# Kernel optimization log

Measured on AMD Instinct MI355X. Metric: run time of the kernel, lower is better.

The kernel has to match this reference:

```python
import jax, jax.numpy as jnp
import numpy as np

RPN_BATCH = 256
ROI_BATCH = 128
IMG = 800.0


def _box_iou(a, b):
    # a: [N,4], b: [G,4] -> [N,G]
    lt = jnp.maximum(a[:, None, :2], b[None, :, :2])
    rb = jnp.minimum(a[:, None, 2:], b[None, :, 2:])
    wh = jnp.clip(rb - lt, 0.0)
    inter = wh[..., 0] * wh[..., 1]
    area_a = (a[:, 2] - a[:, 0]) * (a[:, 3] - a[:, 1])
    area_b = (b[:, 2] - b[:, 0]) * (b[:, 3] - b[:, 1])
    return inter / (area_a[:, None] + area_b[None, :] - inter + 1e-6)


def _encode(a, t):
    wa = a[:, 2] - a[:, 0]
    ha = a[:, 3] - a[:, 1]
    xa = a[:, 0] + 0.5 * wa
    ya = a[:, 1] + 0.5 * ha
    wt = t[:, 2] - t[:, 0]
    ht = t[:, 3] - t[:, 1]
    xt = t[:, 0] + 0.5 * wt
    yt = t[:, 1] + 0.5 * ht
    return jnp.stack(((xt - xa) / wa, (yt - ya) / ha,
                      jnp.log(wt / wa + 1e-6), jnp.log(ht / ha + 1e-6)), axis=1)


def _smooth_l1(x):
    ax = jnp.abs(x)
    return jnp.where(ax < 1.0, 0.5 * x * x, ax - 0.5)


def _rpn_loss_one(scores, deltas, anchors, gt):
    # scores [N,1], deltas [N,4], anchors [N,4], gt [G,4]
    ious = _box_iou(anchors, gt)                 # [N,G]
    max_iou = ious.max(axis=1)
    argmax = ious.argmax(axis=1)
    labels = jnp.full((anchors.shape[0],), -1.0, dtype=scores.dtype)
    labels = jnp.where(max_iou < 0.3, 0.0, labels)
    labels = jnp.where(max_iou > 0.7, 1.0, labels)
    labels = labels.at[jnp.argmax(ious, axis=0)].set(1.0)  # each gt's best anchor is positive
    # deterministic subsampling: keep first K in index order (replaces randperm)
    num_pos = RPN_BATCH // 2
    pos = labels == 1.0
    labels = jnp.where(pos & (jnp.cumsum(pos) > num_pos), -1.0, labels)
    n_pos = jnp.sum(labels == 1.0)
    neg = labels == 0.0
    labels = jnp.where(neg & (jnp.cumsum(neg) > (RPN_BATCH - n_pos)), -1.0, labels)
    mask = (labels != -1.0).astype(scores.dtype)
    logit = scores[:, 0]
    t = jnp.clip(labels, 0.0, 1.0)
    bce = jnp.maximum(logit, 0.0) - logit * t + jnp.log1p(jnp.exp(-jnp.abs(logit)))
    cls = jnp.sum(bce * mask) / jnp.maximum(jnp.sum(mask), 1.0)
    tgt = _encode(anchors, gt[argmax])
    posm = (labels == 1.0).astype(scores.dtype)
    n_posf = jnp.sum(posm)
    reg = jnp.where(n_posf > 0,
                    jnp.sum(_smooth_l1(deltas - tgt) * posm[:, None])
                    / jnp.maximum(n_posf * 4.0, 1.0),
                    0.0)
    return cls + reg


def _det_loss_one(cls_scores, bbox_deltas, proposals, gt, gt_labels):
    # cls_scores [P,C], bbox_deltas [P,4C], proposals [P,4], gt [G,4], gt_labels [G]
    P = proposals.shape[0]
    ious = _box_iou(proposals, gt)
    max_iou = ious.max(axis=1)
    argmax = ious.argmax(axis=1)
    assigned = jnp.where(max_iou >= 0.5, gt_labels[argmax], 0)
    num_pos = ROI_BATCH // 4
    pos = assigned > 0
    pos_rank = jnp.cumsum(pos) - 1
    neg_rank = jnp.cumsum(~pos) - 1
    idx = jnp.arange(P)
    # sort key: first up-to-num_pos positives (index order), then negatives,
    # excess positives pushed to the end -> first ROI_BATCH entries are the sample
    key = jnp.where(pos,
                    jnp.where(pos_rank < num_pos, pos_rank, 2 * P + idx),
                    P + neg_rank)
    sampled = jnp.argsort(key)[:ROI_BATCH]
    t_labels = assigned[sampled]
    matched = gt[argmax[sampled]]
    t_deltas = _encode(proposals[sampled], matched)
    logp = jax.nn.log_softmax(cls_scores[sampled], axis=-1)
    cls = -jnp.mean(jnp.take_along_axis(logp, t_labels[:, None], axis=1)[:, 0])
    pd = bbox_deltas[sampled].reshape(ROI_BATCH, -1, 4)
    preds = pd[jnp.arange(ROI_BATCH), t_labels]  # class-specific deltas
    posm = (t_labels > 0).astype(cls_scores.dtype)
    n_pos = jnp.sum(posm)
    reg = jnp.where(n_pos > 0,
                    jnp.sum(_smooth_l1(preds - t_deltas) * posm[:, None])
                    / jnp.maximum(n_pos * 4.0, 1.0),
                    0.0)
    return cls + reg


def _rand_boxes(k, prefix):
    k1, k2 = jax.random.split(k)
    xy = jax.random.uniform(k1, prefix + (2,)) * (IMG - 130.0)
    wh = jax.random.uniform(k2, prefix + (2,)) * 120.0 + 8.0
    return jnp.concatenate([xy, xy + wh], axis=-1)


def setup_inputs() -> dict:
    B, N, P, G, C = 4, 250000, 1000, 32, 81
    key = jax.random.key(0)
    ks = jax.random.split(key, 8)
    return {
        "rpn_scores": jax.random.normal(ks[0], (B, N, 1), dtype=jnp.float32),
        "rpn_deltas": jax.random.normal(ks[1], (B, N, 4), dtype=jnp.float32) * 0.1,
        "cls_scores": jax.random.normal(ks[2], (B * P, C), dtype=jnp.float32),
        "bbox_deltas": jax.random.normal(ks[3], (B * P, 4 * C), dtype=jnp.float32) * 0.1,
        "anchors": _rand_boxes(ks[4], (N,)),
        "proposals": _rand_boxes(ks[5], (B, P)),
        "gt_boxes": _rand_boxes(ks[6], (B, G)),
        "gt_labels": jax.random.randint(ks[7], (B, G), 1, C, dtype=jnp.int32),
    }


def reference(rpn_scores, rpn_deltas, cls_scores, bbox_deltas,
              anchors, proposals, gt_boxes, gt_labels):
    B, P, _ = proposals.shape
    C = cls_scores.shape[-1]
    cls_b = cls_scores.reshape(B, P, C)
    del_b = bbox_deltas.reshape(B, P, 4 * C)
    rpn = jax.vmap(lambda s, d, g: _rpn_loss_one(s, d, anchors, g))(
        rpn_scores, rpn_deltas, gt_boxes)
    det = jax.vmap(_det_loss_one)(cls_b, del_b, proposals, gt_boxes, gt_labels)
    return jnp.sum(rpn) + jnp.sum(det)
```

## Files before the change

### kernel.cpp

```cpp
#include <hip/hip_runtime.h>
#include <math.h>
#include <stdint.h>

#define B_ 4
#define N_ 250000
#define P_ 1000
#define G_ 32
#define C_ 81
#define RPN_BATCH 256
#define ROI_BATCH 128

#define ABLK 1024
#define NBA ((N_ + ABLK - 1) / ABLK)

__device__ __forceinline__ float iou_one(float a0, float a1, float a2, float a3,
                                         float areaA,
                                         float b0, float b1, float b2, float b3) {
    float ltx = fmaxf(a0, b0), lty = fmaxf(a1, b1);
    float rbx = fminf(a2, b2), rby = fminf(a3, b3);
    float w = fmaxf(rbx - ltx, 0.f), h = fmaxf(rby - lty, 0.f);
    float inter = w * h;
    float areaB = (b2 - b0) * (b3 - b1);
    return inter / (areaA + areaB - inter + 1e-6f);
}

__device__ __forceinline__ unsigned long long shfl_xor_u64(unsigned long long v, int m) {
    unsigned lo = (unsigned)v, hi = (unsigned)(v >> 32);
    lo = __shfl_xor(lo, m);
    hi = __shfl_xor(hi, m);
    return ((unsigned long long)hi << 32) | lo;
}

__device__ __forceinline__ float smooth_l1(float x) {
    float ax = fabsf(x);
    return (ax < 1.f) ? 0.5f * x * x : ax - 0.5f;
}

__global__ void __launch_bounds__(256, 4) rpn_assign(
        const float* __restrict__ anchors, const float* __restrict__ gt_boxes,
        int8_t* __restrict__ labels, int* __restrict__ posCnt, int* __restrict__ negCnt,
        unsigned long long* __restrict__ blockBest,
        float* __restrict__ sums, float* __restrict__ out, int out_size) {
    __shared__ float4 sA[ABLK];
    __shared__ unsigned char sPart[4][ABLK];
    __shared__ int sCnt[8];

    int b = blockIdx.y, tid = threadIdx.x;
    int base = blockIdx.x * ABLK;

    if (blockIdx.x == 0 && b == 0) {
        if (tid < 8) sums[tid] = 0.f;
        for (int i = tid; i < out_size; i += 256) out[i] = 0.f;
    }

    for (int t = tid; t < ABLK; t += 256) {
        int ai = base + t;
        float4 v = make_float4(0.f, 0.f, 0.f, 0.f);
        if (ai < N_) v = ((const float4*)anchors)[ai];
        sA[t] = v;
    }
    __syncthreads();

    int lane = tid & 63, wave = tid >> 6;
    int waveu = __builtin_amdgcn_readfirstlane(wave);

    const float4* gt4 = (const float4*)gt_boxes + b * G_ + waveu * 8;
    float g0[8], g1[8], g2[8], g3[8], gae[8];
#pragma unroll
    for (int j = 0; j < 8; ++j) {
        float4 g = gt4[j];
        g0[j] = g.x; g1[j] = g.y; g2[j] = g.z; g3[j] = g.w;
        gae[j] = (g.z - g.x) * (g.w - g.y) + 1e-6f;
    }

    float bi[8], bd[8]; int bx[8];
#pragma unroll
    for (int j = 0; j < 8; ++j) { bi[j] = 0.f; bd[j] = 1.f; bx[j] = 0; }

    for (int k = 0; k < ABLK / 64; ++k) {
        int a = k * 64 + lane;
        float4 A = sA[a];
        float areaA = (A.z - A.x) * (A.w - A.y);
        int gidx = base + a;
        float acc03 = 1e30f, acc07 = 1e30f;
#pragma unroll
        for (int j = 0; j < 8; ++j) {
            float ltx = fmaxf(A.x, g0[j]), lty = fmaxf(A.y, g1[j]);
            float rbx = fminf(A.z, g2[j]), rby = fminf(A.w, g3[j]);
            float w = fmaxf(rbx - ltx, 0.f), h = fmaxf(rby - lty, 0.f);
            float inter = w * h;
            float d = (areaA + gae[j]) - inter;
            acc03 = fminf(acc03, fmaf(0.3f, d, -inter));
            acc07 = fminf(acc07, fmaf(0.7f, d, -inter));
            float p1 = inter * bd[j], p2 = bi[j] * d;
            if (p1 > p2) { bi[j] = inter; bd[j] = d; bx[j] = gidx; }
        }
        sPart[wave][a] = (unsigned char)(((acc07 < 0.f) ? 2 : 0) | ((acc03 > 0.f) ? 1 : 0));
    }

#pragma unroll
    for (int j = 0; j < 8; ++j) {
        float i_ = bi[j], d_ = bd[j]; int x_ = bx[j];
        for (int m = 32; m >= 1; m >>= 1) {
            float oi = __shfl_xor(i_, m), od = __shfl_xor(d_, m);
            int ox = __shfl_xor(x_, m);
            float pa = oi * d_, pb = i_ * od;
            bool take = (pa > pb) || (pa == pb && ox < x_);
            if (take) { i_ = oi; d_ = od; x_ = ox; }
        }
        if (lane == 0) {
            float iou = i_ / d_;
            unsigned long long pk =
                (((unsigned long long)__float_as_uint(iou)) << 32) |
                (unsigned)(0xFFFFFFFFu - (unsigned)x_);
            blockBest[((size_t)b * G_ + wave * 8 + j) * NBA + blockIdx.x] = pk;
        }
    }
    __syncthreads();

    unsigned u0 = ((const unsigned*)&sPart[0][0])[tid];
    unsigned u1 = ((const unsigned*)&sPart[1][0])[tid];
    unsigned u2 = ((const unsigned*)&sPart[2][0])[tid];
    unsigned u3 = ((const unsigned*)&sPart[3][0])[tid];
    unsigned andb = u0 & u1 & u2 & u3;
    unsigned orb  = u0 | u1 | u2 | u3;
    int gbase = base + tid * 4;
    unsigned outw = 0; int cp = 0, cn = 0;
#pragma unroll
    for (int j = 0; j < 4; ++j) {
        int above = (orb >> (8 * j + 1)) & 1;
        int below = (andb >> (8 * j)) & 1;
        int lab = above ? 1 : (below ? 0 : -1);
        if (gbase + j < N_) { cp += (lab == 1); cn += (lab == 0); }
        outw |= ((unsigned)(unsigned char)(char)lab) << (8 * j);
    }
    if (gbase < N_)
        ((unsigned*)labels)[(((size_t)b * N_ + base) >> 2) + tid] = outw;

    for (int m = 32; m >= 1; m >>= 1) { cp += __shfl_xor(cp, m); cn += __shfl_xor(cn, m); }
    if (lane == 0) { sCnt[wave] = cp; sCnt[4 + wave] = cn; }
    __syncthreads();
    if (tid == 0) {
        posCnt[b * NBA + blockIdx.x] = sCnt[0] + sCnt[1] + sCnt[2] + sCnt[3];
        negCnt[b * NBA + blockIdx.x] = sCnt[4] + sCnt[5] + sCnt[6] + sCnt[7];
    }
}

__global__ void __launch_bounds__(256) rpn_promote_scan(
        const unsigned long long* __restrict__ blockBest, int8_t* __restrict__ labels,
        int* __restrict__ posCnt, int* __restrict__ negCnt,
        int* __restrict__ totPos, int* __restrict__ totNeg) {
    int b = blockIdx.x, tid = threadIdx.x;
    __shared__ int sp[256], sn[256];
    __shared__ unsigned wIdx[G_];

    sp[tid] = (tid < NBA) ? posCnt[b * NBA + tid] : 0;
    sn[tid] = (tid < NBA) ? negCnt[b * NBA + tid] : 0;

    int g = tid >> 3, sub = tid & 7;
    unsigned long long v = 0;
    for (int j = sub; j < NBA; j += 8) {
        unsigned long long x = blockBest[((size_t)b * G_ + g) * NBA + j];
        if (x > v) v = x;
    }
    for (int m = 4; m >= 1; m >>= 1) {
        unsigned long long o = shfl_xor_u64(v, m);
        if (o > v) v = o;
    }
    if (sub == 0) wIdx[g] = 0xFFFFFFFFu - (unsigned)(v & 0xFFFFFFFFull);
    __syncthreads();
    if (tid < G_) {
        unsigned w = wIdx[tid];
        bool first = true;
        for (int j = 0; j < tid; ++j) if (wIdx[j] == w) first = false;
        if (first) {
            size_t li = (size_t)b * N_ + w;
            int8_t old = labels[li];
            labels[li] = 1;
            int blk = (int)(w / ABLK);
            if (old != 1) atomicAdd(&sp[blk], 1);
            if (old == 0) atomicAdd(&sn[blk], -1);
        }
    }
    __syncthreads();

    int vp = sp[tid], vn = sn[tid];
    for (int off = 1; off < 256; off <<= 1) {
        int tp = 0, tn = 0;
        if (tid >= off) { tp = sp[tid - off]; tn = sn[tid - off]; }
        __syncthreads();
        sp[tid] += tp; sn[tid] += tn;
        __syncthreads();
    }
    if (tid < NBA) {
        posCnt[b * NBA + tid] = sp[tid] - vp;
        negCnt[b * NBA + tid] = sn[tid] - vn;
    }
    if (tid == 0) { totPos[b] = sp[255]; totNeg[b] = sn[255]; }
}

__global__ void __launch_bounds__(256) rpn_sample(
        const int8_t* __restrict__ labels, const float* __restrict__ rpn_scores,
        const float* __restrict__ rpn_deltas, const float* __restrict__ anchors,
        const float* __restrict__ gt_boxes,
        const int* __restrict__ posBase, const int* __restrict__ negBase,
        const int* __restrict__ totPos, float* __restrict__ sums) {
    int b = blockIdx.y, tid = threadIdx.x;
    int base = blockIdx.x * ABLK;
    __shared__ float sg[G_ * 4];
    __shared__ int swP[4], swN[4];
    __shared__ float sred[8];
    if (tid < G_ * 4) sg[tid] = gt_boxes[b * G_ * 4 + tid];

    int gbase = base + tid * 4;
    unsigned word = 0xFFFFFFFFu;
    if (gbase < N_)
        word = ((const unsigned*)labels)[(((size_t)b * N_ + base) >> 2) + tid];
    int lab[4]; int cntP = 0, cntN = 0;
#pragma unroll
    for (int j = 0; j < 4; ++j) {
        lab[j] = (int)(char)((word >> (8 * j)) & 0xFF);
        cntP += (lab[j] == 1); cntN += (lab[j] == 0);
    }
    int lane = tid & 63, wave = tid >> 6;
    int ip = cntP, inn = cntN;
    for (int off = 1; off < 64; off <<= 1) {
        int vp = __shfl_up(ip, off), vn = __shfl_up(inn, off);
        if (lane >= off) { ip += vp; inn += vn; }
    }
    if (lane == 63) { swP[wave] = ip; swN[wave] = inn; }
    __syncthreads();
    int bP = 0, bN = 0;
    for (int w = 0; w < wave; ++w) { bP += swP[w]; bN += swN[w]; }
    int pP = posBase[b * NBA + blockIdx.x] + bP + ip - cntP;
    int pN = negBase[b * NBA + blockIdx.x] + bN + inn - cntN;

    int npos = min(totPos[b], RPN_BATCH / 2);
    int negQ = RPN_BATCH - npos;

    float bce = 0.f, regv = 0.f;
#pragma unroll
    for (int j = 0; j < 4; ++j) {
        int i = gbase + j;
        if (i >= N_) break;
        if (lab[j] == 1) {
            int r = pP++;
            if (r < RPN_BATCH / 2) {
                float l = rpn_scores[(size_t)b * N_ + i];
                bce += fmaxf(l, 0.f) - l + log1pf(expf(-fabsf(l)));
                float4 A = ((const float4*)anchors)[i];
                float areaA = (A.z - A.x) * (A.w - A.y);
                float best = -1.f; int am = 0;
                for (int g = 0; g < G_; ++g) {
                    float iou = iou_one(A.x, A.y, A.z, A.w, areaA,
                                        sg[g * 4], sg[g * 4 + 1], sg[g * 4 + 2], sg[g * 4 + 3]);
                    if (iou > best) { best = iou; am = g; }
                }
                float t0 = sg[am * 4], t1 = sg[am * 4 + 1], t2 = sg[am * 4 + 2], t3 = sg[am * 4 + 3];
                float wa = A.z - A.x, ha = A.w - A.y;
                float xa = A.x + 0.5f * wa, ya = A.y + 0.5f * ha;
                float wt = t2 - t0, ht = t3 - t1;
                float xt = t0 + 0.5f * wt, yt = t1 + 0.5f * ht;
                float4 D = ((const float4*)rpn_deltas)[(size_t)b * N_ + i];
                regv += smooth_l1(D.x - (xt - xa) / wa) + smooth_l1(D.y - (yt - ya) / ha) +
                        smooth_l1(D.z - logf(wt / wa + 1e-6f)) + smooth_l1(D.w - logf(ht / ha + 1e-6f));
            }
        } else if (lab[j] == 0) {
            int r = pN++;
            if (r < negQ) {
                float l = rpn_scores[(size_t)b * N_ + i];
                bce += fmaxf(l, 0.f) + log1pf(expf(-fabsf(l)));
            }
        }
    }
    for (int m = 32; m >= 1; m >>= 1) { bce += __shfl_xor(bce, m); regv += __shfl_xor(regv, m); }
    if (lane == 0) { sred[wave] = bce; sred[4 + wave] = regv; }
    __syncthreads();
    if (tid == 0) {
        float sb = sred[0] + sred[1] + sred[2] + sred[3];
        float sr = sred[4] + sred[5] + sred[6] + sred[7];
        if (sb != 0.f) atomicAdd(&sums[b], sb);
        if (sr != 0.f) atomicAdd(&sums[4 + b], sr);
    }
}

__global__ void __launch_bounds__(1024) det_all(
        const float* __restrict__ cls_scores, const float* __restrict__ bbox_deltas,
        const float* __restrict__ proposals, const float* __restrict__ gt_boxes,
        const int* __restrict__ gt_labels, const int* __restrict__ totPos,
        const int* __restrict__ totNeg, const float* __restrict__ sums,
        float* __restrict__ out) {
    int b = blockIdx.x, tid = threadIdx.x;
    int lane = tid & 63, wave = tid >> 6;
    __shared__ float sgt[G_ * 4];
    __shared__ int sgl[G_];
    __shared__ short sassign[P_];
    __shared__ unsigned char sargm[P_];
    __shared__ int sw[16];
    __shared__ int ssamp[ROI_BATCH];
    __shared__ float sRow[ROI_BATCH][C_];
    __shared__ float sM[ROI_BATCH], sLse[ROI_BATCH];
    __shared__ float cacc[2], racc[2];
    if (tid < G_ * 4) sgt[tid] = gt_boxes[b * G_ * 4 + tid];
    if (tid < G_) sgl[tid] = gt_labels[b * G_ + tid];
    __syncthreads();

    int lab = 0;
    if (tid < P_) {
        float4 A = ((const float4*)proposals)[b * P_ + tid];
        float areaA = (A.z - A.x) * (A.w - A.y);
        float best = -1.f; int am = 0;
#pragma unroll 8
        for (int g = 0; g < G_; ++g) {
            float iou = iou_one(A.x, A.y, A.z, A.w, areaA,
                                sgt[g * 4], sgt[g * 4 + 1], sgt[g * 4 + 2], sgt[g * 4 + 3]);
            if (iou > best) { best = iou; am = g; }
        }
        lab = (best >= 0.5f) ? sgl[am] : 0;
        sassign[tid] = (short)lab;
        sargm[tid] = (unsigned char)am;
    }

    int cnt = (tid < P_ && lab > 0) ? 1 : 0;
    int inc = cnt;
    for (int off = 1; off < 64; off <<= 1) {
        int v = __shfl_up(inc, off);
        if (lane >= off) inc += v;
    }
    if (lane == 63) sw[wave] = inc;
    __syncthreads();
    int basew = 0, total = 0;
    for (int w = 0; w < 16; ++w) { if (w < wave) basew += sw[w]; total += sw[w]; }
    int prefix = basew + inc - cnt;
    int npos_kept = min(total, ROI_BATCH / 4);
    int nneg_total = P_ - total;
    if (tid < P_) {
        int slot;
        if (lab > 0)
            slot = (prefix < ROI_BATCH / 4) ? prefix
                 : npos_kept + nneg_total + (prefix - ROI_BATCH / 4);
        else
            slot = npos_kept + (tid - prefix);
        if (slot < ROI_BATCH) ssamp[slot] = tid;
    }
    int np_det = npos_kept + max(0, ROI_BATCH - npos_kept - nneg_total);
    __syncthreads();

    for (int k = 0; k < 8; ++k) {
        int r = wave * 8 + k;
        int s = ssamp[r];
        const float* row = cls_scores + ((size_t)(b * P_ + s)) * C_;
        float v1 = row[lane];
        sRow[r][lane] = v1;
        if (lane < C_ - 64) sRow[r][64 + lane] = row[64 + lane];
    }
    __syncthreads();

    for (int k = 0; k < 8; ++k) {
        int r = wave * 8 + k;
        float v1 = sRow[r][lane];
        float v2 = (lane < C_ - 64) ? sRow[r][64 + lane] : -INFINITY;
        float m = fmaxf(v1, v2);
        for (int mm = 32; mm >= 1; mm >>= 1) m = fmaxf(m, __shfl_xor(m, mm));
        float se = expf(v1 - m) + ((lane < C_ - 64) ? expf(v2 - m) : 0.f);
        for (int mm = 32; mm >= 1; mm >>= 1) se += __shfl_xor(se, mm);
        if (lane == 0) { sM[r] = m; sLse[r] = logf(se); }
    }
    __syncthreads();

    float clsv = 0.f, regv = 0.f;
    if (tid < ROI_BATCH) {
        int s = ssamp[tid];
        int t = sassign[s];
        clsv = -(sRow[tid][t] - sM[tid] - sLse[tid]);
        if (t > 0) {
            int g = sargm[s];
            float4 A = ((const float4*)proposals)[b * P_ + s];
            float t0 = sgt[g * 4], t1 = sgt[g * 4 + 1];
            float t2 = sgt[g * 4 + 2], t3 = sgt[g * 4 + 3];
            float wa = A.z - A.x, ha = A.w - A.y;
            float xa = A.x + 0.5f * wa, ya = A.y + 0.5f * ha;
            float wt = t2 - t0, ht = t3 - t1;
            float xt = t0 + 0.5f * wt, yt = t1 + 0.5f * ht;
            const float4 pd = *(const float4*)(bbox_deltas +
                    ((size_t)(b * P_ + s)) * (4 * C_) + 4 * t);
            regv = smooth_l1(pd.x - (xt - xa) / wa) + smooth_l1(pd.y - (yt - ya) / ha) +
                   smooth_l1(pd.z - logf(wt / wa + 1e-6f)) + smooth_l1(pd.w - logf(ht / ha + 1e-6f));
        }
    }
    if (tid < 128) {
        for (int m = 32; m >= 1; m >>= 1) {
            clsv += __shfl_xor(clsv, m);
            regv += __shfl_xor(regv, m);
        }
        if (lane == 0) { cacc[wave] = clsv; racc[wave] = regv; }
    }
    __syncthreads();
    if (tid == 0) {
        float cls = (cacc[0] + cacc[1]) / (float)ROI_BATCH;
        float reg = (np_det > 0) ? (racc[0] + racc[1]) / fmaxf((float)np_det * 4.f, 1.f) : 0.f;
        int rnp = min(totPos[b], RPN_BATCH / 2);
        int kneg = min(totNeg[b], RPN_BATCH - rnp);
        float rcls = sums[b] / fmaxf((float)(rnp + kneg), 1.f);
        float rreg = (rnp > 0) ? sums[4 + b] / fmaxf((float)rnp * 4.f, 1.f) : 0.f;
        atomicAdd(out, cls + reg + rcls + rreg);
    }
}

extern "C" void kernel_launch(void* const* d_in, const int* in_sizes, int n_in,
                              void* d_out, int out_size, void* d_ws, size_t ws_size,
                              hipStream_t stream) {
    const float* rpn_scores  = (const float*)d_in[0];
    const float* rpn_deltas  = (const float*)d_in[1];
    const float* cls_scores  = (const float*)d_in[2];
    const float* bbox_deltas = (const float*)d_in[3];
    const float* anchors     = (const float*)d_in[4];
    const float* proposals   = (const float*)d_in[5];
    const float* gt_boxes    = (const float*)d_in[6];
    const int*   gt_labels   = (const int*)d_in[7];
    float* out = (float*)d_out;

    char* ws = (char*)d_ws;
    size_t off = 0;
    auto alloc = [&](size_t bytes) -> char* {
        size_t o = (off + 255) & ~(size_t)255;
        off = o + bytes;
        return ws + o;
    };
    int8_t* labels = (int8_t*)alloc((size_t)B_ * N_);
    unsigned long long* blockBest = (unsigned long long*)alloc((size_t)B_ * G_ * NBA * 8);
    int* posCnt = (int*)alloc((size_t)B_ * NBA * 4);
    int* negCnt = (int*)alloc((size_t)B_ * NBA * 4);
    int* totPos = (int*)alloc(B_ * 4);
    int* totNeg = (int*)alloc(B_ * 4);
    float* sums = (float*)alloc(8 * 4);

    rpn_assign<<<dim3(NBA, B_), 256, 0, stream>>>(anchors, gt_boxes, labels,
                                                  posCnt, negCnt, blockBest,
                                                  sums, out, out_size);
    rpn_promote_scan<<<B_, 256, 0, stream>>>(blockBest, labels, posCnt, negCnt,
                                             totPos, totNeg);
    rpn_sample<<<dim3(NBA, B_), 256, 0, stream>>>(labels, rpn_scores, rpn_deltas,
                                                  anchors, gt_boxes, posCnt, negCnt,
                                                  totPos, sums);
    det_all<<<B_, 1024, 0, stream>>>(cls_scores, bbox_deltas, proposals, gt_boxes,
                                     gt_labels, totPos, totNeg, sums, out);
}
```

Before: 159.0 us.

## Fold detection loss into RPN assign kernel as extra blocks, drop det_all launch

```diff
diff --git a/kernel.cpp b/kernel.cpp
--- a/kernel.cpp
+++ b/kernel.cpp
@@ -12,6 +12,7 @@
 
 #define ABLK 1024
 #define NBA ((N_ + ABLK - 1) / ABLK)
+#define DETB 4
 
 __device__ __forceinline__ float iou_one(float a0, float a1, float a2, float a3,
                                          float areaA,
@@ -36,20 +37,154 @@
     return (ax < 1.f) ? 0.5f * x * x : ax - 0.5f;
 }
 
-__global__ void __launch_bounds__(256, 4) rpn_assign(
+__global__ void __launch_bounds__(256, 4) rpn_assign_det(
         const float* __restrict__ anchors, const float* __restrict__ gt_boxes,
+        const int* __restrict__ gt_labels, const float* __restrict__ proposals,
+        const float* __restrict__ cls_scores, const float* __restrict__ bbox_deltas,
         int8_t* __restrict__ labels, int* __restrict__ posCnt, int* __restrict__ negCnt,
-        unsigned long long* __restrict__ blockBest,
-        float* __restrict__ sums, float* __restrict__ out, int out_size) {
+        unsigned long long* __restrict__ blockBest, float* __restrict__ detPart,
+        float* __restrict__ out, int out_size) {
+    int b = blockIdx.y, tid = threadIdx.x;
+    int lane = tid & 63, wave = tid >> 6;
+
+    if (blockIdx.x >= NBA) {
+        int h = blockIdx.x - NBA;
+        __shared__ float sgt[G_ * 4];
+        __shared__ int sgl[G_];
+        __shared__ short sassign[P_];
+        __shared__ unsigned char sargm[P_];
+        __shared__ int ssamp[ROI_BATCH];
+        __shared__ int swd[4];
+        __shared__ float sc[4], srg[4];
+        if (tid < G_ * 4) sgt[tid] = gt_boxes[b * G_ * 4 + tid];
+        if (tid < G_) sgl[tid] = gt_labels[b * G_ + tid];
+        __syncthreads();
+
+        int myPos = 0;
+        int labj[4];
+#pragma unroll
+        for (int j = 0; j < 4; ++j) {
+            int p = tid * 4 + j;
+            int labp = 0, am = 0;
+            if (p < P_) {
+                float4 A = ((const float4*)proposals)[b * P_ + p];
+                float areaA = (A.z - A.x) * (A.w - A.y);
+                float best = -1.f;
+#pragma unroll 8
+                for (int g = 0; g < G_; ++g) {
+                    float iou = iou_one(A.x, A.y, A.z, A.w, areaA,
+                                        sgt[g * 4], sgt[g * 4 + 1], sgt[g * 4 + 2], sgt[g * 4 + 3]);
+                    if (iou > best) { best = iou; am = g; }
+                }
+                labp = (best >= 0.5f) ? sgl[am] : 0;
+                sassign[p] = (short)labp;
+                sargm[p] = (unsigned char)am;
+                labj[j] = labp;
+                myPos += (labp > 0);
+            } else {
+                labj[j] = -1;
+            }
+        }
+
+        int inc = myPos;
+        for (int off = 1; off < 64; off <<= 1) {
+            int v = __shfl_up(inc, off);
+            if (lane >= off) inc += v;
+        }
+        if (lane == 63) swd[wave] = inc;
+        __syncthreads();
+        int basew = 0, total = 0;
+        for (int w = 0; w < 4; ++w) { if (w < wave) basew += swd[w]; total += swd[w]; }
+        int pp = basew + inc - myPos;
+        int npos_kept = min(total, ROI_BATCH / 4);
+        int nneg_total = P_ - total;
+#pragma unroll
+        for (int j = 0; j < 4; ++j) {
+            int p = tid * 4 + j;
+            if (labj[j] < 0) break;
+            int slot;
+            if (labj[j] > 0) {
+                slot = (pp < ROI_BATCH / 4) ? pp : npos_kept + nneg_total + (pp - ROI_BATCH / 4);
+                pp++;
+            } else {
+                slot = npos_kept + (p - pp);
+            }
+            if (slot < ROI_BATCH) ssamp[slot] = p;
+        }
+        int np_det = npos_kept + max(0, ROI_BATCH - npos_kept - nneg_total);
+        __syncthreads();
+
+        int rowBase = h * (ROI_BATCH / DETB) + wave * 8;
+        float clsAcc = 0.f;
+        for (int k = 0; k < 8; k += 2) {
+            int s0 = ssamp[rowBase + k], s1 = ssamp[rowBase + k + 1];
+            const float* r0 = cls_scores + ((size_t)(b * P_ + s0)) * C_;
+            const float* r1 = cls_scores + ((size_t)(b * P_ + s1)) * C_;
+            float a1 = r0[lane], b1 = r1[lane];
+            float a2 = (lane < C_ - 64) ? r0[64 + lane] : -INFINITY;
+            float b2 = (lane < C_ - 64) ? r1[64 + lane] : -INFINITY;
+            float m0 = fmaxf(a1, a2), m1 = fmaxf(b1, b2);
+            for (int mm = 32; mm >= 1; mm >>= 1) {
+                m0 = fmaxf(m0, __shfl_xor(m0, mm));
+                m1 = fmaxf(m1, __shfl_xor(m1, mm));
+            }
+            float e0 = expf(a1 - m0) + ((lane < C_ - 64) ? expf(a2 - m0) : 0.f);
+            float e1 = expf(b1 - m1) + ((lane < C_ - 64) ? expf(b2 - m1) : 0.f);
+            for (int mm = 32; mm >= 1; mm >>= 1) {
+                e0 += __shfl_xor(e0, mm);
+                e1 += __shfl_xor(e1, mm);
+            }
+            int t0 = sassign[s0], t1 = sassign[s1];
+            int q0 = (t0 < 64) ? t0 : t0 - 64;
+            int q1 = (t1 < 64) ? t1 : t1 - 64;
+            float lo0 = __shfl(a1, q0), hi0 = __shfl(a2, q0);
+            float lo1 = __shfl(b1, q1), hi1 = __shfl(b2, q1);
+            float v0 = (t0 < 64) ? lo0 : hi0;
+            float v1 = (t1 < 64) ? lo1 : hi1;
+            if (lane == 0)
+                clsAcc += -(v0 - m0 - logf(e0)) - (v1 - m1 - logf(e1));
+        }
+
+        float regAcc = 0.f;
+        if (lane < 8) {
+            int r = rowBase + lane;
+            int s = ssamp[r];
+            int t = sassign[s];
+            if (t > 0) {
+                int g = sargm[s];
+                float4 A = ((const float4*)proposals)[b * P_ + s];
+                float t0g = sgt[g * 4], t1g = sgt[g * 4 + 1];
+                float t2g = sgt[g * 4 + 2], t3g = sgt[g * 4 + 3];
+                float wa = A.z - A.x, ha = A.w - A.y;
+                float xa = A.x + 0.5f * wa, ya = A.y + 0.5f * ha;
+                float wt = t2g - t0g, ht = t3g - t1g;
+                float xt = t0g + 0.5f * wt, yt = t1g + 0.5f * ht;
+                const float4 pd = *(const float4*)(bbox_deltas +
+                        ((size_t)(b * P_ + s)) * (4 * C_) + 4 * t);
+                regAcc = smooth_l1(pd.x - (xt - xa) / wa) + smooth_l1(pd.y - (yt - ya) / ha) +
+                         smooth_l1(pd.z - logf(wt / wa + 1e-6f)) +
+                         smooth_l1(pd.w - logf(ht / ha + 1e-6f));
+            }
+        }
+        for (int mm = 32; mm >= 1; mm >>= 1) regAcc += __shfl_xor(regAcc, mm);
+        if (lane == 0) { sc[wave] = clsAcc; srg[wave] = regAcc; }
+        __syncthreads();
+        if (tid == 0) {
+            float cp = sc[0] + sc[1] + sc[2] + sc[3];
+            float rp = srg[0] + srg[1] + srg[2] + srg[3];
+            detPart[b * DETB + h] = cp / (float)ROI_BATCH +
+                ((np_det > 0) ? rp / fmaxf((float)np_det * 4.f, 1.f) : 0.f);
+        }
+        return;
+    }
+
     __shared__ float4 sA[ABLK];
     __shared__ unsigned char sPart[4][ABLK];
     __shared__ int sCnt[8];
 
-    int b = blockIdx.y, tid = threadIdx.x;
     int base = blockIdx.x * ABLK;
 
     if (blockIdx.x == 0 && b == 0) {
-        if (tid < 8) sums[tid] = 0.f;
         for (int i = tid; i < out_size; i += 256) out[i] = 0.f;
     }
 
@@ -61,7 +196,6 @@
     }
     __syncthreads();
 
-    int lane = tid & 63, wave = tid >> 6;
     int waveu = __builtin_amdgcn_readfirstlane(wave);
 
     const float4* gt4 = (const float4*)gt_boxes + b * G_ + waveu * 8;
@@ -204,7 +338,8 @@
         const float* __restrict__ rpn_deltas, const float* __restrict__ anchors,
         const float* __restrict__ gt_boxes,
         const int* __restrict__ posBase, const int* __restrict__ negBase,
-        const int* __restrict__ totPos, float* __restrict__ sums) {
+        const int* __restrict__ totPos, const int* __restrict__ totNeg,
+        const float* __restrict__ detPart, float* __restrict__ out) {
     int b = blockIdx.y, tid = threadIdx.x;
     int base = blockIdx.x * ABLK;
     __shared__ float sg[G_ * 4];
@@ -279,131 +414,15 @@
     if (tid == 0) {
         float sb = sred[0] + sred[1] + sred[2] + sred[3];
         float sr = sred[4] + sred[5] + sred[6] + sred[7];
-        if (sb != 0.f) atomicAdd(&sums[b], sb);
-        if (sr != 0.f) atomicAdd(&sums[4 + b], sr);
-    }
-}
-
-__global__ void __launch_bounds__(1024) det_all(
-        const float* __restrict__ cls_scores, const float* __restrict__ bbox_deltas,
-        const float* __restrict__ proposals, const float* __restrict__ gt_boxes,
-        const int* __restrict__ gt_labels, const int* __restrict__ totPos,
-        const int* __restrict__ totNeg, const float* __restrict__ sums,
-        float* __restrict__ out) {
-    int b = blockIdx.x, tid = threadIdx.x;
-    int lane = tid & 63, wave = tid >> 6;
-    __shared__ float sgt[G_ * 4];
-    __shared__ int sgl[G_];
-    __shared__ short sassign[P_];
-    __shared__ unsigned char sargm[P_];
-    __shared__ int sw[16];
-    __shared__ int ssamp[ROI_BATCH];
-    __shared__ float sRow[ROI_BATCH][C_];
-    __shared__ float sM[ROI_BATCH], sLse[ROI_BATCH];
-    __shared__ float cacc[2], racc[2];
-    if (tid < G_ * 4) sgt[tid] = gt_boxes[b * G_ * 4 + tid];
-    if (tid < G_) sgl[tid] = gt_labels[b * G_ + tid];
-    __syncthreads();
-
-    int lab = 0;
-    if (tid < P_) {
-        float4 A = ((const float4*)proposals)[b * P_ + tid];
-        float areaA = (A.z - A.x) * (A.w - A.y);
-        float best = -1.f; int am = 0;
-#pragma unroll 8
-        for (int g = 0; g < G_; ++g) {
-            float iou = iou_one(A.x, A.y, A.z, A.w, areaA,
-                                sgt[g * 4], sgt[g * 4 + 1], sgt[g * 4 + 2], sgt[g * 4 + 3]);
-            if (iou > best) { best = iou; am = g; }
-        }
-        lab = (best >= 0.5f) ? sgl[am] : 0;
-        sassign[tid] = (short)lab;
-        sargm[tid] = (unsigned char)am;
-    }
-
-    int cnt = (tid < P_ && lab > 0) ? 1 : 0;
-    int inc = cnt;
-    for (int off = 1; off < 64; off <<= 1) {
-        int v = __shfl_up(inc, off);
-        if (lane >= off) inc += v;
-    }
-    if (lane == 63) sw[wave] = inc;
-    __syncthreads();
-    int basew = 0, total = 0;
-    for (int w = 0; w < 16; ++w) { if (w < wave) basew += sw[w]; total += sw[w]; }
-    int prefix = basew + inc - cnt;
-    int npos_kept = min(total, ROI_BATCH / 4);
-    int nneg_total = P_ - total;
-    if (tid < P_) {
-        int slot;
-        if (lab > 0)
-            slot = (prefix < ROI_BATCH / 4) ? prefix
-                 : npos_kept + nneg_total + (prefix - ROI_BATCH / 4);
-        else
-            slot = npos_kept + (tid - prefix);
-        if (slot < ROI_BATCH) ssamp[slot] = tid;
-    }
-    int np_det = npos_kept + max(0, ROI_BATCH - npos_kept - nneg_total);
-    __syncthreads();
-
-    for (int k = 0; k < 8; ++k) {
-        int r = wave * 8 + k;
-        int s = ssamp[r];
-        const float* row = cls_scores + ((size_t)(b * P_ + s)) * C_;
-        float v1 = row[lane];
-        sRow[r][lane] = v1;
-        if (lane < C_ - 64) sRow[r][64 + lane] = row[64 + lane];
-    }
-    __syncthreads();
-
-    for (int k = 0; k < 8; ++k) {
-        int r = wave * 8 + k;
-        float v1 = sRow[r][lane];
-        float v2 = (lane < C_ - 64) ? sRow[r][64 + lane] : -INFINITY;
-        float m = fmaxf(v1, v2);
-        for (int mm = 32; mm >= 1; mm >>= 1) m = fmaxf(m, __shfl_xor(m, mm));
-        float se = expf(v1 - m) + ((lane < C_ - 64) ? expf(v2 - m) : 0.f);
-        for (int mm = 32; mm >= 1; mm >>= 1) se += __shfl_xor(se, mm);
-        if (lane == 0) { sM[r] = m; sLse[r] = logf(se); }
-    }
-    __syncthreads();
-
-    float clsv = 0.f, regv = 0.f;
-    if (tid < ROI_BATCH) {
-        int s = ssamp[tid];
-        int t = sassign[s];
-        clsv = -(sRow[tid][t] - sM[tid] - sLse[tid]);
-        if (t > 0) {
-            int g = sargm[s];
-            float4 A = ((const float4*)proposals)[b * P_ + s];
-            float t0 = sgt[g * 4], t1 = sgt[g * 4 + 1];
-            float t2 = sgt[g * 4 + 2], t3 = sgt[g * 4 + 3];
-            float wa = A.z - A.x, ha = A.w - A.y;
-            float xa = A.x + 0.5f * wa, ya = A.y + 0.5f * ha;
-            float wt = t2 - t0, ht = t3 - t1;
-            float xt = t0 + 0.5f * wt, yt = t1 + 0.5f * ht;
-            const float4 pd = *(const float4*)(bbox_deltas +
-                    ((size_t)(b * P_ + s)) * (4 * C_) + 4 * t);
-            regv = smooth_l1(pd.x - (xt - xa) / wa) + smooth_l1(pd.y - (yt - ya) / ha) +
-                   smooth_l1(pd.z - logf(wt / wa + 1e-6f)) + smooth_l1(pd.w - logf(ht / ha + 1e-6f));
-        }
-    }
-    if (tid < 128) {
-        for (int m = 32; m >= 1; m >>= 1) {
-            clsv += __shfl_xor(clsv, m);
-            regv += __shfl_xor(regv, m);
-        }
-        if (lane == 0) { cacc[wave] = clsv; racc[wave] = regv; }
-    }
-    __syncthreads();
-    if (tid == 0) {
-        float cls = (cacc[0] + cacc[1]) / (float)ROI_BATCH;
-        float reg = (np_det > 0) ? (racc[0] + racc[1]) / fmaxf((float)np_det * 4.f, 1.f) : 0.f;
         int rnp = min(totPos[b], RPN_BATCH / 2);
         int kneg = min(totNeg[b], RPN_BATCH - rnp);
-        float rcls = sums[b] / fmaxf((float)(rnp + kneg), 1.f);
-        float rreg = (rnp > 0) ? sums[4 + b] / fmaxf((float)rnp * 4.f, 1.f) : 0.f;
-        atomicAdd(out, cls + reg + rcls + rreg);
+        float denomC = fmaxf((float)(rnp + kneg), 1.f);
+        float contrib = sb / denomC +
+                        ((rnp > 0) ? sr / fmaxf((float)rnp * 4.f, 1.f) : 0.f);
+        if (blockIdx.x == 0)
+            contrib += detPart[b * DETB + 0] + detPart[b * DETB + 1] +
+                       detPart[b * DETB + 2] + detPart[b * DETB + 3];
+        if (contrib != 0.f || blockIdx.x == 0) atomicAdd(out, contrib);
     }
 }
 
@@ -433,16 +452,14 @@
     int* negCnt = (int*)alloc((size_t)B_ * NBA * 4);
     int* totPos = (int*)alloc(B_ * 4);
     int* totNeg = (int*)alloc(B_ * 4);
-    float* sums = (float*)alloc(8 * 4);
-
-    rpn_assign<<<dim3(NBA, B_), 256, 0, stream>>>(anchors, gt_boxes, labels,
-                                                  posCnt, negCnt, blockBest,
-                                                  sums, out, out_size);
+    float* detPart = (float*)alloc(B_ * DETB * 4);
+
+    rpn_assign_det<<<dim3(NBA + DETB, B_), 256, 0, stream>>>(
+            anchors, gt_boxes, gt_labels, proposals, cls_scores, bbox_deltas,
+            labels, posCnt, negCnt, blockBest, detPart, out, out_size);
     rpn_promote_scan<<<B_, 256, 0, stream>>>(blockBest, labels, posCnt, negCnt,
                                              totPos, totNeg);
     rpn_sample<<<dim3(NBA, B_), 256, 0, stream>>>(labels, rpn_scores, rpn_deltas,
                                                   anchors, gt_boxes, posCnt, negCnt,
-                                                  totPos, sums);
-    det_all<<<B_, 1024, 0, stream>>>(cls_scores, bbox_deltas, proposals, gt_boxes,
-                                     gt_labels, totPos, totNeg, sums, out);
-}
+                                                  totPos, totNeg, detPart, out);
+}
```

Measured after the change: 141.6 us. 10.9% less time.
